# Performance work log

Hardware: AMD Instinct MI355X
Metric: run time of the kernel (lower is better)

Reference implementation:

```python
import jax, jax.numpy as jnp
import numpy as np

NHEAD = 8

def layernorm(x, w, b, eps=1e-5):
    mu = jnp.mean(x, axis=-1, keepdims=True)
    var = jnp.mean((x - mu) ** 2, axis=-1, keepdims=True)
    return (x - mu) * jax.lax.rsqrt(var + eps) * w + b

def setup_inputs() -> dict:
    key = jax.random.key(0)
    ks = jax.random.split(key, 3)
    N, in_dim, dim = 2048, 256, 256
    point = jax.random.normal(ks[0], (N, in_dim), dtype=jnp.float32)
    w_qkv = jax.random.normal(ks[1], (in_dim, 3 * dim), dtype=jnp.float32) * (in_dim ** -0.5)
    w_proj = jax.random.normal(ks[2], (dim, dim), dtype=jnp.float32) * (dim ** -0.5)
    return {
        "point": point,
        "w_qkv": w_qkv,
        "w_proj": w_proj,
        "b_proj": jnp.zeros((dim,), jnp.float32),
        "norm1_w": jnp.ones((in_dim,), jnp.float32),
        "norm1_b": jnp.zeros((in_dim,), jnp.float32),
        "norm2_w": jnp.ones((dim,), jnp.float32),
        "norm2_b": jnp.zeros((dim,), jnp.float32),
        "topk": 16,
    }

def reference(point, w_qkv, w_proj, b_proj, norm1_w, norm1_b, norm2_w, norm2_b, topk):
    # Coarse level of QTAttB (i == 0, ONE_BATCH=True)
    N, in_dim = point.shape
    dim = w_proj.shape[0]
    Ch = dim // NHEAD  # per-head channels
    x = layernorm(point, norm1_w, norm1_b)[None]            # [1, N, in_dim]
    qkv = (x @ w_qkv).reshape(1, N, 3, NHEAD, Ch)
    q, k, v = qkv[:, :, 0], qkv[:, :, 1], qkv[:, :, 2]      # [1, N, H, Ch]
    # QK: nlhd,nshd->nlsh ; softmax over key axis s (dim=-2 in torch = axis 2)
    QK = jnp.einsum('blhd,bshd->blsh', q, k)                # [1, N, N, H]
    A = jax.nn.softmax(QK * (Ch ** -0.5), axis=2)
    A_mean = jnp.mean(A, axis=-1)                           # [1, N, N]
    _, topk_idx = jax.lax.top_k(A_mean, topk)               # [1, N, topk]
    message = jnp.einsum('blsh,bshd->blhd', A, v).reshape(1, N, dim)
    message = message @ w_proj + b_proj
    message = v.reshape(1, N, dim) + message
    message = message[0]                                    # squeeze batch
    out = layernorm(message, norm2_w, norm2_b)              # final_message = norm2(message)
    return out, topk_idx[0]
```

## Files before the change

kernel.cpp:

```cpp
#include <hip/hip_runtime.h>

#define NTOK   2048
#define DIM    256
#define NH     8
#define CH     32
#define QB     8
#define TOPK_K 16
#define SCALE  0.17677669529663687f
#define LN_EPS 1e-5f

#define PBL    260
#define PBH    (QB * PBL)
#define PSCALE 16384.f
#define RPSCALE (1.f / 16384.f)

typedef _Float16 h16;
typedef _Float16 h16x8 __attribute__((ext_vector_type(8)));
typedef float    f32x4 __attribute__((ext_vector_type(4)));

#define MFMA16(a, b, c) __builtin_amdgcn_mfma_f32_16x16x32_f16((a), (b), (c), 0, 0, 0)


template<int NT>
__device__ __forceinline__ float block_sum(float v, float* red){
  #pragma unroll
  for (int off = 32; off > 0; off >>= 1) v += __shfl_xor(v, off, 64);
  const int t = threadIdx.x;
  if ((t & 63) == 0) red[t >> 6] = v;
  __syncthreads();
  float s = 0.f;
  #pragma unroll
  for (int w = 0; w < NT/64; w++) s += red[w];
  __syncthreads();
  return s;
}

__global__ __launch_bounds__(256) void reorder_w_kernel(
    const float* __restrict__ src, h16* __restrict__ dst, int ld)
{
  const int b  = blockIdx.x * 4 + (threadIdx.x >> 6);
  const int l  = threadIdx.x & 63;
  const int cg = b >> 3, ks = b & 7;
  h16x8 hi8, lo8;
  #pragma unroll
  for (int j = 0; j < 8; j++){
    const float v = src[(size_t)(ks * 32 + (l >> 4) * 8 + j) * ld + cg * 16 + (l & 15)];
    const h16 h = (h16)v;
    hi8[j] = h;
    lo8[j] = (h16)(v - (float)h);
  }
  *(h16x8*)&dst[(size_t)((cg * 8 + ks) * 2 + 0) * 512 + l * 8] = hi8;
  *(h16x8*)&dst[(size_t)((cg * 8 + ks) * 2 + 1) * 512 + l * 8] = lo8;
}

__global__ __launch_bounds__(1024) void ln_qkv_kernel(
    const float* __restrict__ point,
    const h16*   __restrict__ WF,
    const float* __restrict__ c1,
    const float* __restrict__ c2,
    float* __restrict__ Q,
    h16*   __restrict__ KF,
    h16*   __restrict__ VF,
    float* __restrict__ V)
{
  __shared__ float xs[16][261];
  __shared__ float garr[256], barr[256];
  __shared__ float red[16];
  const int t  = threadIdx.x;
  const int wv = t >> 6;
  const int l  = t & 63;
  const int r  = l & 15;
  const int g  = l >> 4;
  const int l0 = blockIdx.x * 16;

  const float a1 = (t < 256) ? c1[t] : 0.f;
  const float a2 = (t < 256) ? c2[t] : 0.f;
  const float s1 = block_sum<1024>(fabsf(a1), red);
  const float s2 = block_sum<1024>(fabsf(a2), red);
  if (t < 256){ garr[t] = (s1 > s2) ? a1 : a2; barr[t] = (s1 > s2) ? a2 : a1; }
  __syncthreads();

  {
    const float4 x = *(const float4*)&point[(size_t)(l0 + wv) * DIM + 4 * l];
    float s = x.x + x.y + x.z + x.w;
    #pragma unroll
    for (int off = 1; off < 64; off <<= 1) s += __shfl_xor(s, off, 64);
    const float mu = s * (1.f / DIM);
    const float d0 = x.x - mu, d1 = x.y - mu, d2 = x.z - mu, d3 = x.w - mu;
    float ss = d0 * d0 + d1 * d1 + d2 * d2 + d3 * d3;
    #pragma unroll
    for (int off = 1; off < 64; off <<= 1) ss += __shfl_xor(ss, off, 64);
    const float rsd = rsqrtf(ss * (1.f / DIM) + LN_EPS);
    xs[wv][4 * l + 0] = d0 * rsd * garr[4 * l + 0] + barr[4 * l + 0];
    xs[wv][4 * l + 1] = d1 * rsd * garr[4 * l + 1] + barr[4 * l + 1];
    xs[wv][4 * l + 2] = d2 * rsd * garr[4 * l + 2] + barr[4 * l + 2];
    xs[wv][4 * l + 3] = d3 * rsd * garr[4 * l + 3] + barr[4 * l + 3];
  }
  __syncthreads();

  h16x8 ah[8], al[8];
  #pragma unroll
  for (int ks = 0; ks < 8; ks++){
    #pragma unroll
    for (int j = 0; j < 8; j++){
      const float v = xs[r][ks * 32 + 8 * g + j];
      const h16 hi = (h16)v;
      ah[ks][j] = hi;
      al[ks][j] = (h16)(v - (float)hi);
    }
  }

  f32x4 aq = {0.f,0.f,0.f,0.f}, ak = {0.f,0.f,0.f,0.f}, av = {0.f,0.f,0.f,0.f};
  {
    const h16* wf = WF + (size_t)wv * 8192 + (size_t)l * 8;
    #pragma unroll
    for (int ks = 0; ks < 8; ks++){
      const h16x8 bh = *(const h16x8*)(wf + ks * 1024);
      const h16x8 bl = *(const h16x8*)(wf + ks * 1024 + 512);
      aq = MFMA16(ah[ks], bh, aq);
      aq = MFMA16(al[ks], bh, aq);
      aq = MFMA16(ah[ks], bl, aq);
    }
  }
  {
    const h16* wf = WF + (size_t)(16 + wv) * 8192 + (size_t)l * 8;
    #pragma unroll
    for (int ks = 0; ks < 8; ks++){
      const h16x8 bh = *(const h16x8*)(wf + ks * 1024);
      const h16x8 bl = *(const h16x8*)(wf + ks * 1024 + 512);
      ak = MFMA16(ah[ks], bh, ak);
      ak = MFMA16(al[ks], bh, ak);
      ak = MFMA16(ah[ks], bl, ak);
    }
  }
  {
    const h16* wf = WF + (size_t)(32 + wv) * 8192 + (size_t)l * 8;
    #pragma unroll
    for (int ks = 0; ks < 8; ks++){
      const h16x8 bh = *(const h16x8*)(wf + ks * 1024);
      const h16x8 bl = *(const h16x8*)(wf + ks * 1024 + 512);
      av = MFMA16(ah[ks], bh, av);
      av = MFMA16(al[ks], bh, av);
      av = MFMA16(ah[ks], bl, av);
    }
  }

  const int kgb = blockIdx.x;
  const int dc  = wv * 16 + r;
  #pragma unroll
  for (int q4 = 0; q4 < 4; q4++){
    const int tok = 4 * g + q4;
    Q[(size_t)(l0 + tok) * DIM + dc] = aq[q4];
    V[(size_t)(l0 + tok) * DIM + dc] = av[q4];
    {
      const int wh = dc >> 5, gp = (dc & 31) >> 3, jj = dc & 7;
      const float kv = ak[q4];
      const h16 kh2 = (h16)kv;
      const size_t kidx = (size_t)(wh * 128 + kgb) * 1024
                        + (size_t)(gp * 16 + tok) * 8 + jj;
      KF[kidx]       = kh2;
      KF[kidx + 512] = (h16)(kv - (float)kh2);
    }
    {
      const int wh = dc >> 5, hh = (dc & 31) >> 4, cp = dc & 15;
      const int key = l0 + tok;
      const int kb = key >> 5, krem = key & 31, gpp = krem >> 3, jpp = krem & 7;
      VF[(size_t)((wh * 64 + kb) * 2 + hh) * 512
         + (size_t)(gpp * 16 + cp) * 8 + jpp] = (h16)av[q4];
    }
  }
}

__global__ __launch_bounds__(1024) __attribute__((amdgpu_waves_per_eu(4)))
void attn_fused_kernel(
    const float* Q,
    const h16*   __restrict__ KF,
    const h16*   __restrict__ VF,
    float*       msg,
    float*       __restrict__ out_idx)
{
  __shared__ float pbuf[NH * PBH];
  __shared__ float am[QB][NTOK];
  __shared__ float msg_s[2][QB][DIM + 4];
  __shared__ float zbuf[NH * 2 * QB];

  const int t  = threadIdx.x;
  const int wv = t >> 6;
  const int w  = wv & 7;
  const int hf = wv >> 3;
  const int l  = t & 63;
  const int r  = l & 15;
  const int g  = l >> 4;
  const int l0 = blockIdx.x * QB;

  h16x8 qh, ql;
  #pragma unroll
  for (int j = 0; j < 8; j++){ qh[j] = (h16)0.f; ql[j] = (h16)0.f; }
  if (r < QB){
    const float* qp = &Q[(size_t)(l0 + r) * DIM + w * CH + 8 * g];
    const float4 q0 = *(const float4*)qp;
    const float4 q1 = *(const float4*)(qp + 4);
    const float qv[8] = {q0.x, q0.y, q0.z, q0.w, q1.x, q1.y, q1.z, q1.w};
    #pragma unroll
    for (int j = 0; j < 8; j++){
      const float s = qv[j] * SCALE;
      const h16 hi = (h16)s;
      qh[j] = hi;
      ql[j] = (h16)(s - (float)hi);
    }
  }

  const h16* kfw = KF + (size_t)(w * 128) * 1024 + (size_t)l * 8;
  const h16* vfw = VF + (size_t)(w * 64) * 1024 + (size_t)l * 8;

  float zs[4] = {0.f, 0.f, 0.f, 0.f};
  {
    const h16* kf = kfw + (size_t)(hf * 64) * 1024;
    #pragma unroll 2
    for (int kgi = 0; kgi < 64; kgi++){
      const h16x8 bh = *(const h16x8*)(kf + (size_t)kgi * 1024);
      const h16x8 bl = *(const h16x8*)(kf + (size_t)kgi * 1024 + 512);
      f32x4 d = {0.f, 0.f, 0.f, 0.f};
      d = MFMA16(qh, bh, d);
      d = MFMA16(ql, bh, d);
      d = MFMA16(qh, bl, d);
      #pragma unroll
      for (int q4 = 0; q4 < 4; q4++) zs[q4] += __expf(d[q4]);
    }
  }
  #pragma unroll
  for (int q4 = 0; q4 < 4; q4++){
    #pragma unroll
    for (int off = 1; off < 16; off <<= 1) zs[q4] += __shfl_xor(zs[q4], off, 64);
  }
  if (r == 0 && g < 2){
    #pragma unroll
    for (int q4 = 0; q4 < 4; q4++) zbuf[(w * 2 + hf) * QB + 4 * g + q4] = zs[q4];
  }
  __syncthreads();
  float rZ[4];
  #pragma unroll
  for (int q4 = 0; q4 < 4; q4++){
    const int row = 4 * g + q4;
    rZ[q4] = (g < 2) ? 1.f / (zbuf[(w * 2 + 0) * QB + row] + zbuf[(w * 2 + 1) * QB + row])
                     : 0.f;
  }

  f32x4 macc[2];
  #pragma unroll
  for (int dg = 0; dg < 2; dg++) macc[dg] = (f32x4){0.f, 0.f, 0.f, 0.f};

  for (int ti = 0; ti < 8; ti++){
    const int s0 = ti * 256;
    const h16* vft = vfw + (size_t)((ti * 8 + hf * 4) * 2) * 512;

    h16x8 pva[4], pvb[4];
    pva[0] = *(const h16x8*)(vft);
    pvb[0] = *(const h16x8*)(vft + 512);
    pva[1] = *(const h16x8*)(vft + 1024);
    pvb[1] = *(const h16x8*)(vft + 1024 + 512);

    {
      const h16* kft = kfw + (size_t)(ti * 16 + hf * 8) * 1024;
      #pragma unroll 2
      for (int kgi = 0; kgi < 8; kgi++){
        const h16x8 bh = *(const h16x8*)(kft + (size_t)kgi * 1024);
        const h16x8 bl = *(const h16x8*)(kft + (size_t)kgi * 1024 + 512);
        f32x4 d = {0.f, 0.f, 0.f, 0.f};
        d = MFMA16(qh, bh, d);
        d = MFMA16(ql, bh, d);
        d = MFMA16(qh, bl, d);
        if (g < 2){
          const int kbr = hf * 128 + kgi * 16 + r;
          pbuf[w * PBH + (4 * g + 0) * PBL + kbr] = __expf(d[0]) * rZ[0];
          pbuf[w * PBH + (4 * g + 1) * PBL + kbr] = __expf(d[1]) * rZ[1];
          pbuf[w * PBH + (4 * g + 2) * PBL + kbr] = __expf(d[2]) * rZ[2];
          pbuf[w * PBH + (4 * g + 3) * PBL + kbr] = __expf(d[3]) * rZ[3];
        }
      }
    }
    __syncthreads();

    pva[2] = *(const h16x8*)(vft + 2048);
    pvb[2] = *(const h16x8*)(vft + 2048 + 512);
    pva[3] = *(const h16x8*)(vft + 3072);
    pvb[3] = *(const h16x8*)(vft + 3072 + 512);

    #pragma unroll
    for (int st = 0; st < 4; st++){
      h16x8 pa;
      #pragma unroll
      for (int j = 0; j < 8; j++) pa[j] = (h16)0.f;
      if (r < QB){
        const float* pp = &pbuf[w * PBH + r * PBL + hf * 128 + st * 32 + 8 * g];
        const float4 p0 = *(const float4*)pp;
        const float4 p1 = *(const float4*)(pp + 4);
        pa[0] = (h16)(p0.x * PSCALE); pa[1] = (h16)(p0.y * PSCALE);
        pa[2] = (h16)(p0.z * PSCALE); pa[3] = (h16)(p0.w * PSCALE);
        pa[4] = (h16)(p1.x * PSCALE); pa[5] = (h16)(p1.y * PSCALE);
        pa[6] = (h16)(p1.z * PSCALE); pa[7] = (h16)(p1.w * PSCALE);
      }
      macc[0] = MFMA16(pa, pva[st], macc[0]);
      macc[1] = MFMA16(pa, pvb[st], macc[1]);
    }
    #pragma unroll
    for (int rep = 0; rep < 2; rep++){
      const int idx = t + rep * 1024;
      const int q = idx >> 8, key = idx & 255;
      float su = 0.f;
      #pragma unroll
      for (int hh = 0; hh < 8; hh++) su += pbuf[hh * PBH + q * PBL + key];
      am[q][s0 + key] = su * 0.125f;
    }
    __syncthreads();
  }

  if (g < 2){
    #pragma unroll
    for (int dg = 0; dg < 2; dg++)
      #pragma unroll
      for (int q4 = 0; q4 < 4; q4++)
        msg_s[hf][4 * g + q4][w * CH + dg * 16 + r] = macc[dg][q4] * RPSCALE;
  }
  __syncthreads();

  if (wv < QB){
    for (int it = 0; it < TOPK_K; it++){
      float bv = -1e30f; int bi = 0x7fffffff;
      #pragma unroll
      for (int b = 0; b < NTOK / 64; b++){
        const int idx = b * 64 + l;
        const float v = am[wv][idx];
        if (v > bv || (v == bv && idx < bi)){ bv = v; bi = idx; }
      }
      #pragma unroll
      for (int off = 1; off < 64; off <<= 1){
        const float ov = __shfl_xor(bv, off, 64);
        const int   oi = __shfl_xor(bi, off, 64);
        if (ov > bv || (ov == bv && oi < bi)){ bv = ov; bi = oi; }
      }
      if (l == 0){
        out_idx[(l0 + wv) * TOPK_K + it] = (float)bi;
        am[wv][bi] = -1e30f;
      }
    }
  } else {
    const int t2 = t - 512;
    #pragma unroll
    for (int k2 = 0; k2 < 4; k2++){
      const int cell = t2 + 512 * k2;
      const int q = cell >> 8, dcol = cell & 255;
      msg[(size_t)(l0 + q) * DIM + dcol] = msg_s[0][q][dcol] + msg_s[1][q][dcol];
    }
  }
}

__global__ __launch_bounds__(1024) void proj_ln_kernel(
    const float* __restrict__ msg,
    const float* __restrict__ V,
    const h16*   __restrict__ WP,
    const float* __restrict__ b_proj,
    const float* __restrict__ c1,
    const float* __restrict__ c2,
    float* __restrict__ out)
{
  __shared__ float xs[16][261];
  __shared__ float ms2[16][261];
  __shared__ float garr[256], barr[256], bparr[256];
  __shared__ float red[16];
  const int t  = threadIdx.x;
  const int wv = t >> 6;
  const int l  = t & 63;
  const int r  = l & 15;
  const int g  = l >> 4;
  const int l0 = blockIdx.x * 16;

  const float a1 = (t < 256) ? c1[t] : 0.f;
  const float a2 = (t < 256) ? c2[t] : 0.f;
  const float s1 = block_sum<1024>(fabsf(a1), red);
  const float s2 = block_sum<1024>(fabsf(a2), red);
  if (t < 256){
    garr[t]  = (s1 > s2) ? a1 : a2;
    barr[t]  = (s1 > s2) ? a2 : a1;
    bparr[t] = b_proj[t];
  }

  {
    const float4 x = *(const float4*)&msg[(size_t)(l0 + wv) * DIM + 4 * l];
    xs[wv][4 * l + 0] = x.x; xs[wv][4 * l + 1] = x.y;
    xs[wv][4 * l + 2] = x.z; xs[wv][4 * l + 3] = x.w;
  }
  __syncthreads();

  h16x8 ah[8], al[8];
  #pragma unroll
  for (int ks = 0; ks < 8; ks++){
    #pragma unroll
    for (int j = 0; j < 8; j++){
      const float v = xs[r][ks * 32 + 8 * g + j];
      const h16 hi = (h16)v;
      ah[ks][j] = hi;
      al[ks][j] = (h16)(v - (float)hi);
    }
  }

  f32x4 acc = {0.f,0.f,0.f,0.f};
  {
    const h16* wp = WP + (size_t)wv * 8192 + (size_t)l * 8;
    #pragma unroll
    for (int ks = 0; ks < 8; ks++){
      const h16x8 bh = *(const h16x8*)(wp + ks * 1024);
      const h16x8 bl = *(const h16x8*)(wp + ks * 1024 + 512);
      acc = MFMA16(ah[ks], bh, acc);
      acc = MFMA16(al[ks], bh, acc);
      acc = MFMA16(ah[ks], bl, acc);
    }
  }

  const int dc = wv * 16 + r;
  #pragma unroll
  for (int q4 = 0; q4 < 4; q4++){
    const int tok = 4 * g + q4;
    ms2[tok][dc] = acc[q4] + bparr[dc] + V[(size_t)(l0 + tok) * DIM + dc];
  }
  __syncthreads();

  {
    const float x0 = ms2[wv][4 * l + 0], x1 = ms2[wv][4 * l + 1];
    const float x2 = ms2[wv][4 * l + 2], x3 = ms2[wv][4 * l + 3];
    float s = x0 + x1 + x2 + x3;
    #pragma unroll
    for (int off = 1; off < 64; off <<= 1) s += __shfl_xor(s, off, 64);
    const float mu = s * (1.f / DIM);
    const float d0 = x0 - mu, d1 = x1 - mu, d2 = x2 - mu, d3 = x3 - mu;
    float ss = d0 * d0 + d1 * d1 + d2 * d2 + d3 * d3;
    #pragma unroll
    for (int off = 1; off < 64; off <<= 1) ss += __shfl_xor(ss, off, 64);
    const float rsd = rsqrtf(ss * (1.f / DIM) + LN_EPS);
    float4 o;
    o.x = d0 * rsd * garr[4 * l + 0] + barr[4 * l + 0];
    o.y = d1 * rsd * garr[4 * l + 1] + barr[4 * l + 1];
    o.z = d2 * rsd * garr[4 * l + 2] + barr[4 * l + 2];
    o.w = d3 * rsd * garr[4 * l + 3] + barr[4 * l + 3];
    *(float4*)&out[(size_t)(l0 + wv) * DIM + 4 * l] = o;
  }
}

extern "C" void kernel_launch(void* const* d_in, const int* in_sizes, int n_in,
                              void* d_out, int out_size, void* d_ws, size_t ws_size,
                              hipStream_t stream) {
  const float* point  = nullptr;
  const float* w_qkv  = nullptr;
  const float* w_proj = nullptr;
  const float* v256[5] = {nullptr, nullptr, nullptr, nullptr, nullptr};
  int n256 = 0;
  for (int i = 0; i < n_in; i++){
    const int sz = in_sizes[i];
    if      (sz == NTOK * DIM)      point  = (const float*)d_in[i];
    else if (sz == DIM * 3 * DIM)   w_qkv  = (const float*)d_in[i];
    else if (sz == DIM * DIM)       w_proj = (const float*)d_in[i];
    else if (sz == DIM && n256 < 5) v256[n256++] = (const float*)d_in[i];
  }
  const float* b_proj = v256[0];
  const float* n1a    = v256[1];
  const float* n1c    = v256[2];
  const float* n2a    = v256[3];
  const float* n2c    = v256[4];

  float* out     = (float*)d_out;
  float* out_idx = out + (size_t)NTOK * DIM;

  char* ws = (char*)d_ws;
  float* Q   = (float*)(ws);
  float* V   = (float*)(ws + ((size_t)2 << 20));
  h16*   KF  = (h16*)  (ws + ((size_t)4 << 20));
  h16*   VF  = (h16*)  (ws + ((size_t)6 << 20));
  h16*   WF  = (h16*)  (ws + ((size_t)7 << 20));
  h16*   WP  = (h16*)  (ws + ((size_t)7 << 20) + 786432);
  float* msg = Q;

  reorder_w_kernel <<<96, 256, 0, stream>>>(w_qkv,  WF, 768);
  reorder_w_kernel <<<32, 256, 0, stream>>>(w_proj, WP, 256);
  ln_qkv_kernel    <<<NTOK / 16, 1024, 0, stream>>>(point, WF, n1a, n1c, Q, KF, VF, V);
  attn_fused_kernel<<<NTOK / QB, 1024, 0, stream>>>(Q, KF, VF, msg, out_idx);
  proj_ln_kernel   <<<NTOK / 16, 1024, 0, stream>>>(msg, V, WP, b_proj, n2a, n2c, out);
}
```

Before: 190.3 us.

## Split softmax denominator into separate kernel and rebalance QKV projection across blocks

Moves the softmax normalizer pass out of the fused attention kernel into a new z_kernel that writes partial sums, which the attention kernel then reads and combines. The QKV projection kernel is split so each block computes half of the output column groups, doubling grid parallelism. The two weight reorder launches are merged into one, and the head-mean accumulation is vectorized with float4 loads. This costs an extra launch and a global round trip for the partial sums, and it reuses the output buffer as scratch before proj_ln overwrites it.

```diff
diff --git a/kernel.cpp b/kernel.cpp
--- a/kernel.cpp
+++ b/kernel.cpp
@@ -36,11 +36,15 @@
 }
 
 __global__ __launch_bounds__(256) void reorder_w_kernel(
-    const float* __restrict__ src, h16* __restrict__ dst, int ld)
+    const float* __restrict__ src_qkv, const float* __restrict__ src_proj,
+    h16* __restrict__ WF, h16* __restrict__ WP)
 {
-  const int b  = blockIdx.x * 4 + (threadIdx.x >> 6);
+  const int b = blockIdx.x;
+  const float* src; h16* dst; int ld, pair;
+  if (b < 96){ src = src_qkv;  dst = WF; ld = 768; pair = b * 4 + (threadIdx.x >> 6); }
+  else       { src = src_proj; dst = WP; ld = 256; pair = (b - 96) * 4 + (threadIdx.x >> 6); }
   const int l  = threadIdx.x & 63;
-  const int cg = b >> 3, ks = b & 7;
+  const int cg = pair >> 3, ks = pair & 7;
   h16x8 hi8, lo8;
   #pragma unroll
   for (int j = 0; j < 8; j++){
@@ -71,7 +75,9 @@
   const int l  = t & 63;
   const int r  = l & 15;
   const int g  = l >> 4;
-  const int l0 = blockIdx.x * 16;
+  const int tg = blockIdx.x >> 1;
+  const int ch = blockIdx.x & 1;
+  const int l0 = tg * 16;
 
   const float a1 = (t < 256) ? c1[t] : 0.f;
   const float a2 = (t < 256) ? c2[t] : 0.f;
@@ -110,64 +116,100 @@
     }
   }
 
-  f32x4 aq = {0.f,0.f,0.f,0.f}, ak = {0.f,0.f,0.f,0.f}, av = {0.f,0.f,0.f,0.f};
-  {
-    const h16* wf = WF + (size_t)wv * 8192 + (size_t)l * 8;
+  const int kgb = tg;
+  #pragma unroll
+  for (int cgi = 0; cgi < 2; cgi++){
+    if (cgi == 1 && wv >= 8) break;
+    const int cg = ch * 24 + (cgi == 0 ? wv : 16 + wv);
+    f32x4 acc = {0.f, 0.f, 0.f, 0.f};
+    const h16* wf = WF + (size_t)cg * 8192 + (size_t)l * 8;
     #pragma unroll
     for (int ks = 0; ks < 8; ks++){
       const h16x8 bh = *(const h16x8*)(wf + ks * 1024);
       const h16x8 bl = *(const h16x8*)(wf + ks * 1024 + 512);
-      aq = MFMA16(ah[ks], bh, aq);
-      aq = MFMA16(al[ks], bh, aq);
-      aq = MFMA16(ah[ks], bl, aq);
-    }
-  }
+      acc = MFMA16(ah[ks], bh, acc);
+      acc = MFMA16(al[ks], bh, acc);
+      acc = MFMA16(ah[ks], bl, acc);
+    }
+    const int typ = cg >> 4;
+    const int c0  = (cg & 15) * 16 + r;
+    #pragma unroll
+    for (int q4 = 0; q4 < 4; q4++){
+      const int tok = 4 * g + q4;
+      if (typ == 0){
+        Q[(size_t)(l0 + tok) * DIM + c0] = acc[q4];
+      } else if (typ == 1){
+        const int wh = c0 >> 5, gp = (c0 & 31) >> 3, jj = c0 & 7;
+        const float kv = acc[q4];
+        const h16 kh2 = (h16)kv;
+        const size_t kidx = (size_t)(wh * 128 + kgb) * 1024
+                          + (size_t)(gp * 16 + tok) * 8 + jj;
+        KF[kidx]       = kh2;
+        KF[kidx + 512] = (h16)(kv - (float)kh2);
+      } else {
+        V[(size_t)(l0 + tok) * DIM + c0] = acc[q4];
+        const int wh = c0 >> 5, hh = (c0 & 31) >> 4, cp = c0 & 15;
+        const int key = l0 + tok;
+        const int kb = key >> 5, krem = key & 31, gpp = krem >> 3, jpp = krem & 7;
+        VF[(size_t)((wh * 64 + kb) * 2 + hh) * 512
+           + (size_t)(gpp * 16 + cp) * 8 + jpp] = (h16)acc[q4];
+      }
+    }
+  }
+}
+
+__global__ __launch_bounds__(1024) void z_kernel(
+    const float* __restrict__ Q,
+    const h16*   __restrict__ KF,
+    float*       __restrict__ Zp)
+{
+  const int t  = threadIdx.x;
+  const int wv = t >> 6;
+  const int w  = wv & 7;
+  const int sh = wv >> 3;
+  const int l  = t & 63;
+  const int r  = l & 15;
+  const int g  = l >> 4;
+  const int tg = blockIdx.x >> 1;
+  const int hb = blockIdx.x & 1;
+
+  h16x8 qh, ql;
   {
-    const h16* wf = WF + (size_t)(16 + wv) * 8192 + (size_t)l * 8;
-    #pragma unroll
-    for (int ks = 0; ks < 8; ks++){
-      const h16x8 bh = *(const h16x8*)(wf + ks * 1024);
-      const h16x8 bl = *(const h16x8*)(wf + ks * 1024 + 512);
-      ak = MFMA16(ah[ks], bh, ak);
-      ak = MFMA16(al[ks], bh, ak);
-      ak = MFMA16(ah[ks], bl, ak);
-    }
-  }
-  {
-    const h16* wf = WF + (size_t)(32 + wv) * 8192 + (size_t)l * 8;
-    #pragma unroll
-    for (int ks = 0; ks < 8; ks++){
-      const h16x8 bh = *(const h16x8*)(wf + ks * 1024);
-      const h16x8 bl = *(const h16x8*)(wf + ks * 1024 + 512);
-      av = MFMA16(ah[ks], bh, av);
-      av = MFMA16(al[ks], bh, av);
-      av = MFMA16(ah[ks], bl, av);
-    }
-  }
-
-  const int kgb = blockIdx.x;
-  const int dc  = wv * 16 + r;
+    const float* qp = &Q[(size_t)(tg * 16 + r) * DIM + w * CH + 8 * g];
+    const float4 q0 = *(const float4*)qp;
+    const float4 q1 = *(const float4*)(qp + 4);
+    const float qv[8] = {q0.x, q0.y, q0.z, q0.w, q1.x, q1.y, q1.z, q1.w};
+    #pragma unroll
+    for (int j = 0; j < 8; j++){
+      const float s = qv[j] * SCALE;
+      const h16 hi = (h16)s;
+      qh[j] = hi;
+      ql[j] = (h16)(s - (float)hi);
+    }
+  }
+
+  const h16* kf = KF + (size_t)(w * 128 + hb * 64 + sh * 32) * 1024 + (size_t)l * 8;
+  float zs[4] = {0.f, 0.f, 0.f, 0.f};
+  #pragma unroll 2
+  for (int kgi = 0; kgi < 32; kgi++){
+    const h16x8 bh = *(const h16x8*)(kf + (size_t)kgi * 1024);
+    const h16x8 bl = *(const h16x8*)(kf + (size_t)kgi * 1024 + 512);
+    f32x4 d = {0.f, 0.f, 0.f, 0.f};
+    d = MFMA16(qh, bh, d);
+    d = MFMA16(ql, bh, d);
+    d = MFMA16(qh, bl, d);
+    #pragma unroll
+    for (int q4 = 0; q4 < 4; q4++) zs[q4] += __expf(d[q4]);
+  }
   #pragma unroll
   for (int q4 = 0; q4 < 4; q4++){
-    const int tok = 4 * g + q4;
-    Q[(size_t)(l0 + tok) * DIM + dc] = aq[q4];
-    V[(size_t)(l0 + tok) * DIM + dc] = av[q4];
-    {
-      const int wh = dc >> 5, gp = (dc & 31) >> 3, jj = dc & 7;
-      const float kv = ak[q4];
-      const h16 kh2 = (h16)kv;
-      const size_t kidx = (size_t)(wh * 128 + kgb) * 1024
-                        + (size_t)(gp * 16 + tok) * 8 + jj;
-      KF[kidx]       = kh2;
-      KF[kidx + 512] = (h16)(kv - (float)kh2);
-    }
-    {
-      const int wh = dc >> 5, hh = (dc & 31) >> 4, cp = dc & 15;
-      const int key = l0 + tok;
-      const int kb = key >> 5, krem = key & 31, gpp = krem >> 3, jpp = krem & 7;
-      VF[(size_t)((wh * 64 + kb) * 2 + hh) * 512
-         + (size_t)(gpp * 16 + cp) * 8 + jpp] = (h16)av[q4];
-    }
+    #pragma unroll
+    for (int off = 1; off < 16; off <<= 1) zs[q4] += __shfl_xor(zs[q4], off, 64);
+  }
+  if (r == 0){
+    #pragma unroll
+    for (int q4 = 0; q4 < 4; q4++)
+      Zp[(size_t)((hb * 2 + sh) * NH + w) * NTOK + tg * 16 + 4 * g + q4] = zs[q4];
   }
 }
 
@@ -176,13 +218,14 @@
     const float* Q,
     const h16*   __restrict__ KF,
     const h16*   __restrict__ VF,
+    const float* __restrict__ Zp,
     float*       msg,
     float*       __restrict__ out_idx)
 {
   __shared__ float pbuf[NH * PBH];
   __shared__ float am[QB][NTOK];
   __shared__ float msg_s[2][QB][DIM + 4];
-  __shared__ float zbuf[NH * 2 * QB];
+  __shared__ float zbuf[NH * QB];
 
   const int t  = threadIdx.x;
   const int wv = t >> 6;
@@ -210,41 +253,23 @@
     }
   }
 
+  if (t < 64){
+    const int h = t >> 3, q = t & 7;
+    float z = 0.f;
+    #pragma unroll
+    for (int p = 0; p < 4; p++) z += Zp[(size_t)(p * NH + h) * NTOK + l0 + q];
+    zbuf[t] = z;
+  }
+  __syncthreads();
+  float rZ[4];
+  #pragma unroll
+  for (int q4 = 0; q4 < 4; q4++){
+    const int row = 4 * g + q4;
+    rZ[q4] = (g < 2) ? 1.f / zbuf[w * QB + row] : 0.f;
+  }
+
   const h16* kfw = KF + (size_t)(w * 128) * 1024 + (size_t)l * 8;
   const h16* vfw = VF + (size_t)(w * 64) * 1024 + (size_t)l * 8;
-
-  float zs[4] = {0.f, 0.f, 0.f, 0.f};
-  {
-    const h16* kf = kfw + (size_t)(hf * 64) * 1024;
-    #pragma unroll 2
-    for (int kgi = 0; kgi < 64; kgi++){
-      const h16x8 bh = *(const h16x8*)(kf + (size_t)kgi * 1024);
-      const h16x8 bl = *(const h16x8*)(kf + (size_t)kgi * 1024 + 512);
-      f32x4 d = {0.f, 0.f, 0.f, 0.f};
-      d = MFMA16(qh, bh, d);
-      d = MFMA16(ql, bh, d);
-      d = MFMA16(qh, bl, d);
-      #pragma unroll
-      for (int q4 = 0; q4 < 4; q4++) zs[q4] += __expf(d[q4]);
-    }
-  }
-  #pragma unroll
-  for (int q4 = 0; q4 < 4; q4++){
-    #pragma unroll
-    for (int off = 1; off < 16; off <<= 1) zs[q4] += __shfl_xor(zs[q4], off, 64);
-  }
-  if (r == 0 && g < 2){
-    #pragma unroll
-    for (int q4 = 0; q4 < 4; q4++) zbuf[(w * 2 + hf) * QB + 4 * g + q4] = zs[q4];
-  }
-  __syncthreads();
-  float rZ[4];
-  #pragma unroll
-  for (int q4 = 0; q4 < 4; q4++){
-    const int row = 4 * g + q4;
-    rZ[q4] = (g < 2) ? 1.f / (zbuf[(w * 2 + 0) * QB + row] + zbuf[(w * 2 + 1) * QB + row])
-                     : 0.f;
-  }
 
   f32x4 macc[2];
   #pragma unroll
@@ -303,14 +328,16 @@
       macc[0] = MFMA16(pa, pva[st], macc[0]);
       macc[1] = MFMA16(pa, pvb[st], macc[1]);
     }
-    #pragma unroll
-    for (int rep = 0; rep < 2; rep++){
-      const int idx = t + rep * 1024;
-      const int q = idx >> 8, key = idx & 255;
-      float su = 0.f;
+    if (t < 512){
+      const int q = t >> 6, k4 = (t & 63) * 4;
+      float4 su = make_float4(0.f, 0.f, 0.f, 0.f);
       #pragma unroll
-      for (int hh = 0; hh < 8; hh++) su += pbuf[hh * PBH + q * PBL + key];
-      am[q][s0 + key] = su * 0.125f;
+      for (int hh = 0; hh < 8; hh++){
+        const float4 v = *(const float4*)&pbuf[hh * PBH + q * PBL + k4];
+        su.x += v.x; su.y += v.y; su.z += v.z; su.w += v.w;
+      }
+      *(float4*)&am[q][s0 + k4] =
+          make_float4(su.x * 0.125f, su.y * 0.125f, su.z * 0.125f, su.w * 0.125f);
     }
     __syncthreads();
   }
@@ -404,7 +431,7 @@
     }
   }
 
-  f32x4 acc = {0.f,0.f,0.f,0.f};
+  f32x4 acc = {0.f, 0.f, 0.f, 0.f};
   {
     const h16* wp = WP + (size_t)wv * 8192 + (size_t)l * 8;
     #pragma unroll
@@ -478,10 +505,11 @@
   h16*   WF  = (h16*)  (ws + ((size_t)7 << 20));
   h16*   WP  = (h16*)  (ws + ((size_t)7 << 20) + 786432);
   float* msg = Q;
-
-  reorder_w_kernel <<<96, 256, 0, stream>>>(w_qkv,  WF, 768);
-  reorder_w_kernel <<<32, 256, 0, stream>>>(w_proj, WP, 256);
-  ln_qkv_kernel    <<<NTOK / 16, 1024, 0, stream>>>(point, WF, n1a, n1c, Q, KF, VF, V);
-  attn_fused_kernel<<<NTOK / QB, 1024, 0, stream>>>(Q, KF, VF, msg, out_idx);
+  float* Zp  = out;
+
+  reorder_w_kernel <<<128,       256,  0, stream>>>(w_qkv, w_proj, WF, WP);
+  ln_qkv_kernel    <<<256,       1024, 0, stream>>>(point, WF, n1a, n1c, Q, KF, VF, V);
+  z_kernel         <<<256,       1024, 0, stream>>>(Q, KF, Zp);
+  attn_fused_kernel<<<NTOK / QB, 1024, 0, stream>>>(Q, KF, VF, Zp, msg, out_idx);
   proj_ln_kernel   <<<NTOK / 16, 1024, 0, stream>>>(msg, V, WP, b_proj, n2a, n2c, out);
 }
```

Result: faster. 181.0 us (median of 3 runs) (-4.9%).
